# Kernel optimization log

Hardware: AMD Instinct MI355X
Metric: run time of the kernel (lower is better)

The kernel has to match this reference:

```python
import jax, jax.numpy as jnp
import numpy as np

N_ATOMS = 51200
N_MOL = 512
FEAT = 384


def setup_inputs() -> dict:
    key = jax.random.key(0)
    ks = jax.random.split(key, 20)
    s = 0.05  # small random weights instead of the degenerate zero-init
    inp = {
        "node_feats": jax.random.normal(ks[0], (N_ATOMS, FEAT), jnp.float32),
        "energy": jax.random.normal(ks[1], (N_MOL,), jnp.float32),
        "forces": jax.random.normal(ks[2], (N_ATOMS, 3), jnp.float32),
        "stress": jax.random.normal(ks[3], (N_MOL, 3, 3), jnp.float32),
        "W1": jax.random.normal(ks[4], (64, 256), jnp.float32) * s,
        "b1": jnp.zeros((64,), jnp.float32),
        "W2": jax.random.normal(ks[5], (16, 64), jnp.float32) * s,
        "b2": jnp.zeros((16,), jnp.float32),
        "W3": jax.random.normal(ks[6], (1, 16), jnp.float32) * s,
        "b3": jnp.zeros((1,), jnp.float32),
        "W1f": jax.random.normal(ks[7], (64, 256), jnp.float32) * s,
        "b1f": jnp.zeros((64,), jnp.float32),
        "W2f": jax.random.normal(ks[8], (16, 64), jnp.float32) * s,
        "b2f": jnp.zeros((16,), jnp.float32),
        "W3f": jax.random.normal(ks[9], (1, 16), jnp.float32) * s,
        "b3f": jnp.zeros((1,), jnp.float32),
        "S_uncert": jnp.zeros((1,), jnp.float32),
        # atom -> molecule segment ids (sorted, every molecule non-empty)
        "batch_idx": jnp.repeat(jnp.arange(N_MOL, dtype=jnp.int64), N_ATOMS // N_MOL),
    }
    return inp


def _mlp(x, W1, b1, W2, b2, W3, b3):
    h = jax.nn.silu(x @ W1.T + b1)
    h = jax.nn.silu(h @ W2.T + b2)
    return h @ W3.T + b3  # [N, 1]


def reference(node_feats, energy, forces, stress,
              W1, b1, W2, b2, W3, b3,
              W1f, b1f, W2f, b2f, W3f, b3f,
              S_uncert, batch_idx):
    # concat first 128 and last 128 feature channels -> [N, 256]
    nf = jnp.concatenate([node_feats[:, :128], node_feats[:, -128:]], axis=1)

    # E head: faithfully zeroed out and replaced by constant 0.6
    e_stds = jnp.exp(_mlp(nf, W1, b1, W2, b2, W3, b3))[:, 0] * 0 + 0.6  # [N]
    # F head
    f_u = jnp.exp(_mlp(nf, W1f, b1f, W2f, b2f, W3f, b3f))[:, 0] * 0.1   # [N]
    force_uncert = jnp.stack([f_u, f_u, f_u], axis=-1)                  # [N, 3]
    # stress uncert: constant 0.1/16 (S_uncert term zeroed, kept faithfully)
    stress_uncert = jnp.ones_like(stress) * jnp.exp(S_uncert[0]) * 0 + 0.1 / 16

    # per-molecule mean of e_stds via segment sums (scatter_add in torch)
    eu_sum = jax.ops.segment_sum(e_stds, batch_idx, num_segments=N_MOL)
    n_atoms = jax.ops.segment_sum(jnp.ones_like(e_stds), batch_idx, num_segments=N_MOL)
    energy_uncert = eu_sum / n_atoms  # [n_mol]

    return (energy, forces, stress, energy_uncert, force_uncert, stress_uncert)
```

## Files before the change

kernel.cpp:

```cpp
#include <hip/hip_runtime.h>
#include <hip/hip_bf16.h>

#define N_ATOMS 51200

#define OUT_FUNC 159232

typedef __attribute__((ext_vector_type(4))) float f32x4;
typedef __attribute__((ext_vector_type(4))) unsigned u32x4;
typedef __attribute__((ext_vector_type(8))) short s16x8;

constexpr int BLK = 256;

__device__ __forceinline__ unsigned pack2(float lo, float hi) {
    return __builtin_amdgcn_perm(__float_as_uint(hi), __float_as_uint(lo), 0x07060302);
}
__device__ __forceinline__ s16x8 pack8(f32x4 lo, f32x4 hi) {
    union { u32x4 u; s16x8 s; } c;
    c.u.x = pack2(lo.x, lo.y); c.u.y = pack2(lo.z, lo.w);
    c.u.z = pack2(hi.x, hi.y); c.u.w = pack2(hi.z, hi.w);
    return c.s;
}
__device__ __forceinline__ short bftrunc(float x) {
    return (short)(__float_as_uint(x) >> 16);
}
__device__ __forceinline__ float silu_(float v) { return v / (1.0f + __expf(-v)); }

#define VMCNT4()  asm volatile("s_waitcnt vmcnt(4)" ::: "memory")
#define VMCNT0()  asm volatile("s_waitcnt vmcnt(0)" ::: "memory")
#define RAWBAR()  asm volatile("s_barrier" ::: "memory")

__global__ __launch_bounds__(BLK, 5) void funcert_kernel(
    const float* __restrict__ nf,
    const float* __restrict__ energy,
    const float* __restrict__ forces,
    const float* __restrict__ stress,
    const float* __restrict__ W1f, const float* __restrict__ b1f,
    const float* __restrict__ W2f, const float* __restrict__ b2f,
    const float* __restrict__ W3f, const float* __restrict__ b3f,
    float* __restrict__ out)
{
    const int t   = threadIdx.x;
    const int gid = blockIdx.x * BLK + t;

    __shared__ float Xe[3][64 * 32];
    __shared__ short H1s[64 * 64];

    const int lane  = t & 63;
    const int w     = t >> 6;
    const int g     = lane >> 4;
    const int col   = lane & 15;
    const int abase = blockIdx.x * 64;
    const int ch    = w * 16 + col;

    const int rloc = lane >> 3;
    const int sl   = lane & 7;

    #define GLD_E(buf, e)                                                    \
        { _Pragma("unroll")                                                  \
          for (int i = 0; i < 2; ++i) {                                      \
              const int br = w * 16 + i * 8;                                 \
              const float* src = nf + (size_t)(abase + br + rloc) * 384      \
                                 + (32 * (e) + ((e) >= 4 ? 128 : 0))         \
                                 + ((sl ^ rloc) << 2);                       \
              __builtin_amdgcn_global_load_lds(                              \
                  (const __attribute__((address_space(1))) void*)src,        \
                  (__attribute__((address_space(3))) void*)((buf) + br * 32),\
                  16, 0, 0);                                                 \
          } }

    #define WQ_E(dst, e)                                                     \
        { const float* p = W1f + ch * 256 + (e) * 32 + g * 8;                \
          dst[0] = *(const f32x4*)p;                                         \
          dst[1] = *(const f32x4*)(p + 4); }

    #define COMP_E(buf, wvv)                                                 \
        { const s16x8 wf = pack8(wvv[0], wvv[1]);                            \
          _Pragma("unroll")                                                  \
          for (int mt = 0; mt < 4; ++mt) {                                   \
              const int row = mt * 16 + col;                                 \
              const int s0  = (2 * g) ^ (row & 7);                           \
              const f32x4 lo = *(const f32x4*)((buf) + row * 32 + (s0)      * 4); \
              const f32x4 hi = *(const f32x4*)((buf) + row * 32 + (s0 ^ 1)  * 4); \
              acc[mt] = __builtin_amdgcn_mfma_f32_16x16x32_bf16(             \
                          pack8(lo, hi), wf, acc[mt], 0, 0, 0);              \
          } }

    f32x4 cv = {0.f, 0.f, 0.f, 0.f}; int co = -1;
    if (gid < 40960) {
        co = gid;
        if      (gid < 128)   { cv = ((const f32x4*)energy)[gid]; }
        else if (gid < 38528) { cv = ((const f32x4*)forces)[gid - 128]; }
        else if (gid < 39680) { cv = ((const f32x4*)stress)[gid - 38528]; }
        else if (gid < 39808) { cv = (f32x4){0.6f, 0.6f, 0.6f, 0.6f}; }
        else { cv = (f32x4){0.00625f, 0.00625f, 0.00625f, 0.00625f}; co = gid + 38400; }
    }

    const float b1v = b1f[ch];
    f32x4 wvA[2], wvB[2], wvC[2];
    GLD_E(Xe[0], 0);  WQ_E(wvA, 0);
    GLD_E(Xe[1], 1);  WQ_E(wvB, 1);

    f32x4 acc[4];
    #pragma unroll
    for (int mt = 0; mt < 4; ++mt) acc[mt] = (f32x4){0.f, 0.f, 0.f, 0.f};

    VMCNT4(); RAWBAR();  GLD_E(Xe[2], 2); WQ_E(wvC, 2);  COMP_E(Xe[0], wvA);
    VMCNT4(); RAWBAR();  GLD_E(Xe[0], 3); WQ_E(wvA, 3);  COMP_E(Xe[1], wvB);
    VMCNT4(); RAWBAR();  GLD_E(Xe[1], 4); WQ_E(wvB, 4);  COMP_E(Xe[2], wvC);
    VMCNT4(); RAWBAR();  GLD_E(Xe[2], 5); WQ_E(wvC, 5);  COMP_E(Xe[0], wvA);
    VMCNT4(); RAWBAR();  GLD_E(Xe[0], 6); WQ_E(wvA, 6);  COMP_E(Xe[1], wvB);
    VMCNT4(); RAWBAR();  GLD_E(Xe[1], 7); WQ_E(wvB, 7);  COMP_E(Xe[2], wvC);
    VMCNT4(); RAWBAR();                                  COMP_E(Xe[0], wvA);
    VMCNT0(); RAWBAR();                                  COMP_E(Xe[1], wvB);

    #pragma unroll
    for (int mt = 0; mt < 4; ++mt) {
        #pragma unroll
        for (int r = 0; r < 4; ++r) {
            const int atom = mt * 16 + g * 4 + r;
            H1s[atom * 64 + ch] = bftrunc(silu_(acc[mt][r] + b1v));
        }
    }
    __syncthreads();

    s16x8 w2frag[2];
    #pragma unroll
    for (int ks = 0; ks < 2; ++ks) {
        const float* p = W2f + col * 64 + ks * 32 + g * 8;
        w2frag[ks] = pack8(*(const f32x4*)p, *(const f32x4*)(p + 4));
    }
    const int arow = w * 16 + col;
    f32x4 a2 = {0.f, 0.f, 0.f, 0.f};
    #pragma unroll
    for (int ks = 0; ks < 2; ++ks) {
        const s16x8 af = *(const s16x8*)(H1s + arow * 64 + ks * 32 + g * 8);
        a2 = __builtin_amdgcn_mfma_f32_16x16x32_bf16(af, w2frag[ks], a2, 0, 0, 0);
    }

    const float b2v = b2f[col];
    const float w3v = W3f[col];
    float y[4];
    #pragma unroll
    for (int r = 0; r < 4; ++r)
        y[r] = silu_(a2[r] + b2v) * w3v;
    #pragma unroll
    for (int m = 1; m < 16; m <<= 1) {
        #pragma unroll
        for (int r = 0; r < 4; ++r)
            y[r] += __shfl_xor(y[r], m, 64);
    }
    const float b3v = b3f[0];
    float fu[4];
    #pragma unroll
    for (int r = 0; r < 4; ++r)
        fu[r] = __expf(y[r] + b3v) * 0.1f;

    if (col < 12) {
        const int a_ = col / 3, c = col - a_ * 3;
        const float v = (a_ == 0) ? fu[0] : (a_ == 1) ? fu[1] : (a_ == 2) ? fu[2] : fu[3];
        const int atom = w * 16 + g * 4 + a_;
        out[OUT_FUNC + 3 * (abase + atom) + c] = v;
    }

    if (co >= 0) ((f32x4*)out)[co] = cv;
}

extern "C" void kernel_launch(void* const* d_in, const int* in_sizes, int n_in,
                              void* d_out, int out_size, void* d_ws, size_t ws_size,
                              hipStream_t stream) {
    const float* nf     = (const float*)d_in[0];
    const float* energy = (const float*)d_in[1];
    const float* forces = (const float*)d_in[2];
    const float* stress = (const float*)d_in[3];
    const float* W1f    = (const float*)d_in[10];
    const float* b1f    = (const float*)d_in[11];
    const float* W2f    = (const float*)d_in[12];
    const float* b2f    = (const float*)d_in[13];
    const float* W3f    = (const float*)d_in[14];
    const float* b3f    = (const float*)d_in[15];
    float* out = (float*)d_out;

    dim3 grid(N_ATOMS / 64);
    funcert_kernel<<<grid, BLK, 0, stream>>>(nf, energy, forces, stress,
                                             W1f, b1f, W2f, b2f, W3f, b3f, out);
}
```

Baseline: 19.90 us.

## Deepen LDS staging ring to four buffers and preload all W1 fragments

The staging ring for the first-layer matmul grows from three to four LDS buffers, so three async feature-tile loads are in flight before compute starts. All W1 weight slices are loaded into registers and packed to bf16 up front, rather than interleaved per stage. The goal is to hide more global-load latency behind the MFMA work. In exchange, LDS use and register pressure rise, and the launch-bounds occupancy hint drops from 5 to 4 blocks per CU.

```diff
diff --git a/kernel.cpp b/kernel.cpp
--- a/kernel.cpp
+++ b/kernel.cpp
@@ -26,10 +26,11 @@
 __device__ __forceinline__ float silu_(float v) { return v / (1.0f + __expf(-v)); }
 
 #define VMCNT4()  asm volatile("s_waitcnt vmcnt(4)" ::: "memory")
+#define VMCNT2()  asm volatile("s_waitcnt vmcnt(2)" ::: "memory")
 #define VMCNT0()  asm volatile("s_waitcnt vmcnt(0)" ::: "memory")
 #define RAWBAR()  asm volatile("s_barrier" ::: "memory")
 
-__global__ __launch_bounds__(BLK, 5) void funcert_kernel(
+__global__ __launch_bounds__(BLK, 4) void funcert_kernel(
     const float* __restrict__ nf,
     const float* __restrict__ energy,
     const float* __restrict__ forces,
@@ -42,7 +43,7 @@
     const int t   = threadIdx.x;
     const int gid = blockIdx.x * BLK + t;
 
-    __shared__ float Xe[3][64 * 32];
+    __shared__ float Xe[4][64 * 32];
     __shared__ short H1s[64 * 64];
 
     const int lane  = t & 63;
@@ -68,19 +69,13 @@
                   16, 0, 0);                                                 \
           } }
 
-    #define WQ_E(dst, e)                                                     \
-        { const float* p = W1f + ch * 256 + (e) * 32 + g * 8;                \
-          dst[0] = *(const f32x4*)p;                                         \
-          dst[1] = *(const f32x4*)(p + 4); }
-
-    #define COMP_E(buf, wvv)                                                 \
-        { const s16x8 wf = pack8(wvv[0], wvv[1]);                            \
-          _Pragma("unroll")                                                  \
+    #define COMP_E(buf, wf)                                                  \
+        { _Pragma("unroll")                                                  \
           for (int mt = 0; mt < 4; ++mt) {                                   \
               const int row = mt * 16 + col;                                 \
               const int s0  = (2 * g) ^ (row & 7);                           \
-              const f32x4 lo = *(const f32x4*)((buf) + row * 32 + (s0)      * 4); \
-              const f32x4 hi = *(const f32x4*)((buf) + row * 32 + (s0 ^ 1)  * 4); \
+              const f32x4 lo = *(const f32x4*)((buf) + row * 32 + (s0)     * 4); \
+              const f32x4 hi = *(const f32x4*)((buf) + row * 32 + (s0 ^ 1) * 4); \
               acc[mt] = __builtin_amdgcn_mfma_f32_16x16x32_bf16(             \
                           pack8(lo, hi), wf, acc[mt], 0, 0, 0);              \
           } }
@@ -95,23 +90,35 @@
         else { cv = (f32x4){0.00625f, 0.00625f, 0.00625f, 0.00625f}; co = gid + 38400; }
     }
 
+    f32x4 wv[16];
+    #pragma unroll
+    for (int e = 0; e < 8; ++e) {
+        const float* p = W1f + ch * 256 + e * 32 + g * 8;
+        wv[2 * e]     = *(const f32x4*)p;
+        wv[2 * e + 1] = *(const f32x4*)(p + 4);
+    }
     const float b1v = b1f[ch];
-    f32x4 wvA[2], wvB[2], wvC[2];
-    GLD_E(Xe[0], 0);  WQ_E(wvA, 0);
-    GLD_E(Xe[1], 1);  WQ_E(wvB, 1);
+
+    GLD_E(Xe[0], 0);
+    GLD_E(Xe[1], 1);
+    GLD_E(Xe[2], 2);
+
+    s16x8 wfp[8];
+    #pragma unroll
+    for (int e = 0; e < 8; ++e) wfp[e] = pack8(wv[2 * e], wv[2 * e + 1]);
 
     f32x4 acc[4];
     #pragma unroll
     for (int mt = 0; mt < 4; ++mt) acc[mt] = (f32x4){0.f, 0.f, 0.f, 0.f};
 
-    VMCNT4(); RAWBAR();  GLD_E(Xe[2], 2); WQ_E(wvC, 2);  COMP_E(Xe[0], wvA);
-    VMCNT4(); RAWBAR();  GLD_E(Xe[0], 3); WQ_E(wvA, 3);  COMP_E(Xe[1], wvB);
-    VMCNT4(); RAWBAR();  GLD_E(Xe[1], 4); WQ_E(wvB, 4);  COMP_E(Xe[2], wvC);
-    VMCNT4(); RAWBAR();  GLD_E(Xe[2], 5); WQ_E(wvC, 5);  COMP_E(Xe[0], wvA);
-    VMCNT4(); RAWBAR();  GLD_E(Xe[0], 6); WQ_E(wvA, 6);  COMP_E(Xe[1], wvB);
-    VMCNT4(); RAWBAR();  GLD_E(Xe[1], 7); WQ_E(wvB, 7);  COMP_E(Xe[2], wvC);
-    VMCNT4(); RAWBAR();                                  COMP_E(Xe[0], wvA);
-    VMCNT0(); RAWBAR();                                  COMP_E(Xe[1], wvB);
+    VMCNT4(); RAWBAR();  GLD_E(Xe[3], 3);  COMP_E(Xe[0], wfp[0]);
+    VMCNT4(); RAWBAR();  GLD_E(Xe[0], 4);  COMP_E(Xe[1], wfp[1]);
+    VMCNT4(); RAWBAR();  GLD_E(Xe[1], 5);  COMP_E(Xe[2], wfp[2]);
+    VMCNT4(); RAWBAR();  GLD_E(Xe[2], 6);  COMP_E(Xe[3], wfp[3]);
+    VMCNT4(); RAWBAR();  GLD_E(Xe[3], 7);  COMP_E(Xe[0], wfp[4]);
+    VMCNT4(); RAWBAR();                    COMP_E(Xe[1], wfp[5]);
+    VMCNT2(); RAWBAR();                    COMP_E(Xe[2], wfp[6]);
+    VMCNT0(); RAWBAR();                    COMP_E(Xe[3], wfp[7]);
 
     #pragma unroll
     for (int mt = 0; mt < 4; ++mt) {
```

After: 22.75 us. 14.4% more time.

## Halve atoms per block to 32 and deepen LDS ring to four buffers

Applied to the files above, without the earlier changes.

Each block now handles 32 atoms instead of 64, which doubles the grid to 1600 blocks. Each wave issues one global-to-LDS load per stage, and the staging ring grows from three to four buffers with a matching vmcnt wait. The aim is more blocks in flight and deeper prefetch to hide HBM latency. In exchange, every block reloads the W1 weights for half as many atoms, and two of the four waves sit idle during the second layer. The constant-copy guard stays tied to gid < 40960, so it still works with the larger grid.

```diff
diff --git a/kernel.cpp b/kernel.cpp
--- a/kernel.cpp
+++ b/kernel.cpp
@@ -10,6 +10,7 @@
 typedef __attribute__((ext_vector_type(8))) short s16x8;
 
 constexpr int BLK = 256;
+constexpr int TA  = 32;
 
 __device__ __forceinline__ unsigned pack2(float lo, float hi) {
     return __builtin_amdgcn_perm(__float_as_uint(hi), __float_as_uint(lo), 0x07060302);
@@ -25,7 +26,7 @@
 }
 __device__ __forceinline__ float silu_(float v) { return v / (1.0f + __expf(-v)); }
 
-#define VMCNT4()  asm volatile("s_waitcnt vmcnt(4)" ::: "memory")
+#define VMCNT3()  asm volatile("s_waitcnt vmcnt(3)" ::: "memory")
 #define VMCNT0()  asm volatile("s_waitcnt vmcnt(0)" ::: "memory")
 #define RAWBAR()  asm volatile("s_barrier" ::: "memory")
 
@@ -42,31 +43,28 @@
     const int t   = threadIdx.x;
     const int gid = blockIdx.x * BLK + t;
 
-    __shared__ float Xe[3][64 * 32];
-    __shared__ short H1s[64 * 64];
+    __shared__ float Xe[4][TA * 32];
+    __shared__ short H1s[TA * 64];
 
     const int lane  = t & 63;
     const int w     = t >> 6;
     const int g     = lane >> 4;
     const int col   = lane & 15;
-    const int abase = blockIdx.x * 64;
+    const int abase = blockIdx.x * TA;
     const int ch    = w * 16 + col;
 
     const int rloc = lane >> 3;
     const int sl   = lane & 7;
 
     #define GLD_E(buf, e)                                                    \
-        { _Pragma("unroll")                                                  \
-          for (int i = 0; i < 2; ++i) {                                      \
-              const int br = w * 16 + i * 8;                                 \
-              const float* src = nf + (size_t)(abase + br + rloc) * 384      \
-                                 + (32 * (e) + ((e) >= 4 ? 128 : 0))         \
-                                 + ((sl ^ rloc) << 2);                       \
-              __builtin_amdgcn_global_load_lds(                              \
-                  (const __attribute__((address_space(1))) void*)src,        \
-                  (__attribute__((address_space(3))) void*)((buf) + br * 32),\
-                  16, 0, 0);                                                 \
-          } }
+        { const int br = w * 8;                                              \
+          const float* src = nf + (size_t)(abase + br + rloc) * 384          \
+                             + (32 * (e) + ((e) >= 4 ? 128 : 0))             \
+                             + ((sl ^ rloc) << 2);                           \
+          __builtin_amdgcn_global_load_lds(                                  \
+              (const __attribute__((address_space(1))) void*)src,            \
+              (__attribute__((address_space(3))) void*)((buf) + br * 32),    \
+              16, 0, 0); }
 
     #define WQ_E(dst, e)                                                     \
         { const float* p = W1f + ch * 256 + (e) * 32 + g * 8;                \
@@ -76,11 +74,11 @@
     #define COMP_E(buf, wvv)                                                 \
         { const s16x8 wf = pack8(wvv[0], wvv[1]);                            \
           _Pragma("unroll")                                                  \
-          for (int mt = 0; mt < 4; ++mt) {                                   \
+          for (int mt = 0; mt < 2; ++mt) {                                   \
               const int row = mt * 16 + col;                                 \
               const int s0  = (2 * g) ^ (row & 7);                           \
-              const f32x4 lo = *(const f32x4*)((buf) + row * 32 + (s0)      * 4); \
-              const f32x4 hi = *(const f32x4*)((buf) + row * 32 + (s0 ^ 1)  * 4); \
+              const f32x4 lo = *(const f32x4*)((buf) + row * 32 + (s0)     * 4); \
+              const f32x4 hi = *(const f32x4*)((buf) + row * 32 + (s0 ^ 1) * 4); \
               acc[mt] = __builtin_amdgcn_mfma_f32_16x16x32_bf16(             \
                           pack8(lo, hi), wf, acc[mt], 0, 0, 0);              \
           } }
@@ -100,21 +98,21 @@
     GLD_E(Xe[0], 0);  WQ_E(wvA, 0);
     GLD_E(Xe[1], 1);  WQ_E(wvB, 1);
 
-    f32x4 acc[4];
-    #pragma unroll
-    for (int mt = 0; mt < 4; ++mt) acc[mt] = (f32x4){0.f, 0.f, 0.f, 0.f};
+    f32x4 acc[2];
+    acc[0] = (f32x4){0.f, 0.f, 0.f, 0.f};
+    acc[1] = (f32x4){0.f, 0.f, 0.f, 0.f};
 
-    VMCNT4(); RAWBAR();  GLD_E(Xe[2], 2); WQ_E(wvC, 2);  COMP_E(Xe[0], wvA);
-    VMCNT4(); RAWBAR();  GLD_E(Xe[0], 3); WQ_E(wvA, 3);  COMP_E(Xe[1], wvB);
-    VMCNT4(); RAWBAR();  GLD_E(Xe[1], 4); WQ_E(wvB, 4);  COMP_E(Xe[2], wvC);
-    VMCNT4(); RAWBAR();  GLD_E(Xe[2], 5); WQ_E(wvC, 5);  COMP_E(Xe[0], wvA);
-    VMCNT4(); RAWBAR();  GLD_E(Xe[0], 6); WQ_E(wvA, 6);  COMP_E(Xe[1], wvB);
-    VMCNT4(); RAWBAR();  GLD_E(Xe[1], 7); WQ_E(wvB, 7);  COMP_E(Xe[2], wvC);
-    VMCNT4(); RAWBAR();                                  COMP_E(Xe[0], wvA);
-    VMCNT0(); RAWBAR();                                  COMP_E(Xe[1], wvB);
+    VMCNT3(); RAWBAR();  GLD_E(Xe[2], 2); WQ_E(wvC, 2);  COMP_E(Xe[0], wvA);
+    VMCNT3(); RAWBAR();  GLD_E(Xe[3], 3); WQ_E(wvA, 3);  COMP_E(Xe[1], wvB);
+    VMCNT3(); RAWBAR();  GLD_E(Xe[0], 4); WQ_E(wvB, 4);  COMP_E(Xe[2], wvC);
+    VMCNT3(); RAWBAR();  GLD_E(Xe[1], 5); WQ_E(wvC, 5);  COMP_E(Xe[3], wvA);
+    VMCNT3(); RAWBAR();  GLD_E(Xe[2], 6); WQ_E(wvA, 6);  COMP_E(Xe[0], wvB);
+    VMCNT3(); RAWBAR();  GLD_E(Xe[3], 7); WQ_E(wvB, 7);  COMP_E(Xe[1], wvC);
+    VMCNT3(); RAWBAR();                                  COMP_E(Xe[2], wvA);
+    VMCNT0(); RAWBAR();                                  COMP_E(Xe[3], wvB);
 
     #pragma unroll
-    for (int mt = 0; mt < 4; ++mt) {
+    for (int mt = 0; mt < 2; ++mt) {
         #pragma unroll
         for (int r = 0; r < 4; ++r) {
             const int atom = mt * 16 + g * 4 + r;
@@ -123,43 +121,45 @@
     }
     __syncthreads();
 
-    s16x8 w2frag[2];
-    #pragma unroll
-    for (int ks = 0; ks < 2; ++ks) {
-        const float* p = W2f + col * 64 + ks * 32 + g * 8;
-        w2frag[ks] = pack8(*(const f32x4*)p, *(const f32x4*)(p + 4));
-    }
-    const int arow = w * 16 + col;
-    f32x4 a2 = {0.f, 0.f, 0.f, 0.f};
-    #pragma unroll
-    for (int ks = 0; ks < 2; ++ks) {
-        const s16x8 af = *(const s16x8*)(H1s + arow * 64 + ks * 32 + g * 8);
-        a2 = __builtin_amdgcn_mfma_f32_16x16x32_bf16(af, w2frag[ks], a2, 0, 0, 0);
-    }
+    if (w < 2) {
+        s16x8 w2frag[2];
+        #pragma unroll
+        for (int ks = 0; ks < 2; ++ks) {
+            const float* p = W2f + col * 64 + ks * 32 + g * 8;
+            w2frag[ks] = pack8(*(const f32x4*)p, *(const f32x4*)(p + 4));
+        }
+        const int arow = w * 16 + col;
+        f32x4 a2 = {0.f, 0.f, 0.f, 0.f};
+        #pragma unroll
+        for (int ks = 0; ks < 2; ++ks) {
+            const s16x8 af = *(const s16x8*)(H1s + arow * 64 + ks * 32 + g * 8);
+            a2 = __builtin_amdgcn_mfma_f32_16x16x32_bf16(af, w2frag[ks], a2, 0, 0, 0);
+        }
 
-    const float b2v = b2f[col];
-    const float w3v = W3f[col];
-    float y[4];
-    #pragma unroll
-    for (int r = 0; r < 4; ++r)
-        y[r] = silu_(a2[r] + b2v) * w3v;
-    #pragma unroll
-    for (int m = 1; m < 16; m <<= 1) {
+        const float b2v = b2f[col];
+        const float w3v = W3f[col];
+        float y[4];
         #pragma unroll
         for (int r = 0; r < 4; ++r)
-            y[r] += __shfl_xor(y[r], m, 64);
-    }
-    const float b3v = b3f[0];
-    float fu[4];
-    #pragma unroll
-    for (int r = 0; r < 4; ++r)
-        fu[r] = __expf(y[r] + b3v) * 0.1f;
+            y[r] = silu_(a2[r] + b2v) * w3v;
+        #pragma unroll
+        for (int m = 1; m < 16; m <<= 1) {
+            #pragma unroll
+            for (int r = 0; r < 4; ++r)
+                y[r] += __shfl_xor(y[r], m, 64);
+        }
+        const float b3v = b3f[0];
+        float fu[4];
+        #pragma unroll
+        for (int r = 0; r < 4; ++r)
+            fu[r] = __expf(y[r] + b3v) * 0.1f;
 
-    if (col < 12) {
-        const int a_ = col / 3, c = col - a_ * 3;
-        const float v = (a_ == 0) ? fu[0] : (a_ == 1) ? fu[1] : (a_ == 2) ? fu[2] : fu[3];
-        const int atom = w * 16 + g * 4 + a_;
-        out[OUT_FUNC + 3 * (abase + atom) + c] = v;
+        if (col < 12) {
+            const int a_ = col / 3, c = col - a_ * 3;
+            const float v = (a_ == 0) ? fu[0] : (a_ == 1) ? fu[1] : (a_ == 2) ? fu[2] : fu[3];
+            const int atom = w * 16 + g * 4 + a_;
+            out[OUT_FUNC + 3 * (abase + atom) + c] = v;
+        }
     }
 
     if (co >= 0) ((f32x4*)out)[co] = cv;
@@ -180,7 +180,7 @@
     const float* b3f    = (const float*)d_in[15];
     float* out = (float*)d_out;
 
-    dim3 grid(N_ATOMS / 64);
+    dim3 grid(N_ATOMS / TA);
     funcert_kernel<<<grid, BLK, 0, stream>>>(nf, energy, forces, stress,
                                              W1f, b1f, W2f, b2f, W3f, b3f, out);
 }
```

After: 23.78 us. 1.19x slower.
